# Optimization experiments

Hardware: AMD Instinct MI355X
Metric: run time of the kernel (lower is better)

## Reference

```python
import jax, jax.numpy as jnp
import numpy as np

NUM_NODES = 100000
NUM_EDGES = 1600000
IN_DIM, HID_DIM, OUT_DIM = 128, 128, 70


def gcn_conv(x, edge_index, W, b):
    """PyG-style GCNConv: linear transform, add self-loops, symmetric
    degree-normalized scatter-add aggregation, plus bias."""
    n = x.shape[0]
    xw = x @ W  # [N, D_out]
    src, dst = edge_index[0], edge_index[1]  # messages flow src -> dst
    loop = jnp.arange(n)
    src = jnp.concatenate([src, loop])
    dst = jnp.concatenate([dst, loop])
    # degree computed at target nodes (with self-loops), edge weight 1
    deg = jax.ops.segment_sum(jnp.ones_like(dst, dtype=xw.dtype), dst,
                              num_segments=n)
    dinv = jnp.where(deg > 0, jax.lax.rsqrt(deg), 0.0)
    norm = dinv[src] * dinv[dst]  # [E+N]
    msgs = xw[src] * norm[:, None]  # [E+N, D_out] gathered messages
    out = jax.ops.segment_sum(msgs, dst, num_segments=n)
    return out + b


def setup_inputs() -> dict:
    key = jax.random.key(0)
    k = jax.random.split(key, 6)
    x = jax.random.normal(k[0], (NUM_NODES, IN_DIM), dtype=jnp.float32)
    edge_index = jax.random.randint(k[1], (2, NUM_EDGES), 0, NUM_NODES,
                                    dtype=jnp.int64)
    # Glorot-style init for weights, zero bias (PyG default)
    W1 = jax.random.normal(k[2], (IN_DIM, HID_DIM), dtype=jnp.float32) / np.sqrt(IN_DIM)
    b1 = jnp.zeros((HID_DIM,), dtype=jnp.float32)
    W2 = jax.random.normal(k[3], (HID_DIM, OUT_DIM), dtype=jnp.float32) / np.sqrt(HID_DIM)
    b2 = jnp.zeros((OUT_DIM,), dtype=jnp.float32)
    return {"x": x, "edge_index": edge_index, "W1": W1, "b1": b1,
            "W2": W2, "b2": b2}


def reference(x, edge_index, W1, b1, W2, b2):
    h = gcn_conv(x, edge_index, W1, b1)
    h = jax.nn.relu(h)
    # dropout(p=0.5) is identity in eval mode
    out = gcn_conv(h, edge_index, W2, b2)
    return out
```

## Files before the change

### kernel.cpp

```cpp
#include <hip/hip_runtime.h>
#include <hip/hip_bf16.h>


#define BSH 8
#define BCHUNK 8192
#define BCAP 8192

typedef __attribute__((ext_vector_type(8))) short short8;
typedef __attribute__((ext_vector_type(4))) float float4v;
typedef __attribute__((ext_vector_type(2))) float float2v;

__device__ __forceinline__ float bf_lo(unsigned u) { return __uint_as_float(u << 16); }
__device__ __forceinline__ float bf_hi(unsigned u) { return __uint_as_float(u & 0xffff0000u); }
__device__ __forceinline__ float bf2f(unsigned short h) {
    return __uint_as_float((unsigned)h << 16);
}
__device__ __forceinline__ unsigned short f2bf(float f) {
    unsigned u = __float_as_uint(f);
    u += 0x7fff + ((u >> 16) & 1);
    return (unsigned short)(u >> 16);
}
__device__ __forceinline__ void acc8(float* acc, uint4 m) {
    acc[0] += bf_lo(m.x); acc[1] += bf_hi(m.x);
    acc[2] += bf_lo(m.y); acc[3] += bf_hi(m.y);
    acc[4] += bf_lo(m.z); acc[5] += bf_hi(m.z);
    acc[6] += bf_lo(m.w); acc[7] += bf_hi(m.w);
}

__global__ void k_bucket_scatter(const int* __restrict__ src, const int* __restrict__ dst,
                                 int* __restrict__ bwcur,
                                 unsigned long long* __restrict__ tmp, int E, int nb) {
    __shared__ int lh[512];
    __shared__ int lb[512];
    int t = threadIdx.x;
    for (int j = t; j < nb; j += 256) lh[j] = 0;
    __syncthreads();
    int e0 = blockIdx.x * BCHUNK;
    int e1 = min(E, e0 + BCHUNK);
    for (int e = e0 + t; e < e1; e += 256) atomicAdd(&lh[dst[e] >> BSH], 1);
    __syncthreads();
    for (int j = t; j < nb; j += 256) {
        int c = lh[j];
        lb[j] = c ? atomicAdd(&bwcur[j], c) : 0;
        lh[j] = 0;
    }
    __syncthreads();
    for (int e = e0 + t; e < e1; e += 256) {
        int d = dst[e];
        int b = d >> BSH;
        int o = atomicAdd(&lh[b], 1);
        int pos = lb[b] + o;
        if (pos < BCAP)
            tmp[(size_t)b * BCAP + pos] =
                ((unsigned long long)(unsigned)d << 32) | (unsigned)src[e];
    }
}

__global__ void k_bucket_finalize(const unsigned long long* __restrict__ tmp,
                                  const int* __restrict__ bwcur,
                                  int* __restrict__ deg, float* __restrict__ dinv,
                                  int* __restrict__ rs, int* __restrict__ csr, int N) {
    __shared__ int cnt[256];
    __shared__ int sc[256];
    int b = blockIdx.x;
    int t = threadIdx.x;
    int e0 = b * BCAP;
    int e1 = e0 + min(bwcur[b], BCAP);
    cnt[t] = 0;
    __syncthreads();
    for (int e = e0 + t; e < e1; e += 256) {
        int d = (int)(tmp[e] >> 32);
        atomicAdd(&cnt[d & 255], 1);
    }
    __syncthreads();
    int c = cnt[t];
    sc[t] = c;
    __syncthreads();
    for (int off = 1; off < 256; off <<= 1) {
        int add = (t >= off) ? sc[t - off] : 0;
        __syncthreads();
        sc[t] += add;
        __syncthreads();
    }
    int excl = sc[t] - c;
    __syncthreads();
    sc[t] = excl;
    int node = (b << BSH) + t;
    if (node < N) {
        deg[node] = c;
        dinv[node] = rsqrtf((float)(c + 1));
        rs[node] = e0 + excl;
    }
    cnt[t] = 0;
    __syncthreads();
    for (int e = e0 + t; e < e1; e += 256) {
        unsigned long long p = tmp[e];
        int j = ((int)(p >> 32)) & 255;
        int o = atomicAdd(&cnt[j], 1);
        csr[e0 + sc[j] + o] = (int)(p & 0xffffffffu);
    }
}

__global__ void k_prep_w(const float* __restrict__ W1, const float* __restrict__ W2,
                         unsigned short* __restrict__ w1th, unsigned short* __restrict__ w1tl,
                         unsigned short* __restrict__ w2th, unsigned short* __restrict__ w2tl) {
    int i = blockIdx.x * blockDim.x + threadIdx.x;
    if (i < 128 * 128) {
        int col = i % 128, k = i / 128;
        float w = W1[k * 128 + col];
        unsigned short h = f2bf(w);
        w1th[(size_t)col * 128 + k] = h;
        w1tl[(size_t)col * 128 + k] = f2bf(w - bf2f(h));
    } else if (i < 128 * 128 + 80 * 128) {
        int j = i - 128 * 128;
        int col = j % 80, k = j / 80;
        float w = (col < 70) ? W2[k * 70 + col] : 0.f;
        unsigned short h = f2bf(w);
        w2th[(size_t)col * 128 + k] = h;
        w2tl[(size_t)col * 128 + k] = f2bf(w - bf2f(h));
    }
}

template <int DOUT, int OSTRIDE, int NT>
__global__ __launch_bounds__(256, 3) void k_gemm_mfma(
        const float* __restrict__ X, const unsigned short* __restrict__ Wth,
        const unsigned short* __restrict__ Wtl,
        const float* __restrict__ dinv, unsigned short* __restrict__ Y, int n) {
    __shared__ short xs_h[64][136];
    __shared__ short xs_l[64][136];
    int t = threadIdx.x;
    int lane = t & 63, wave = t >> 6;
    int m16 = lane & 15, quad = lane >> 4;
    int r0 = blockIdx.x * 64;

    short8 bh[2][4], bl[2][4];
    int nt0 = wave, nt1 = wave + 4;
#pragma unroll
    for (int i = 0; i < 2; i++) {
        int nt = i ? nt1 : nt0;
        if (nt >= NT) continue;
        int col = nt * 16 + m16;
#pragma unroll
        for (int kc = 0; kc < 4; kc++) {
            bh[i][kc] = *(const short8*)&Wth[(size_t)col * 128 + kc * 32 + quad * 8];
            bl[i][kc] = *(const short8*)&Wtl[(size_t)col * 128 + kc * 32 + quad * 8];
        }
    }

    for (int p = t; p < 64 * 32; p += 256) {
        int row = p >> 5;
        int k4 = p & 31;
        int gr = r0 + row;
        if (gr >= n) gr = n - 1;
        float4v xv = __builtin_nontemporal_load(
            (const float4v*)(X + (size_t)gr * 128 + 4 * k4));
        unsigned short h0 = f2bf(xv.x), h1 = f2bf(xv.y);
        unsigned short h2 = f2bf(xv.z), h3 = f2bf(xv.w);
        unsigned short l0 = f2bf(xv.x - bf2f(h0)), l1 = f2bf(xv.y - bf2f(h1));
        unsigned short l2 = f2bf(xv.z - bf2f(h2)), l3 = f2bf(xv.w - bf2f(h3));
        *(uint2*)&xs_h[row][4 * k4] =
            make_uint2((unsigned)h0 | ((unsigned)h1 << 16), (unsigned)h2 | ((unsigned)h3 << 16));
        *(uint2*)&xs_l[row][4 * k4] =
            make_uint2((unsigned)l0 | ((unsigned)l1 << 16), (unsigned)l2 | ((unsigned)l3 << 16));
    }
    __syncthreads();

    float4v acc[2][4];
#pragma unroll
    for (int i = 0; i < 2; i++)
#pragma unroll
        for (int ms = 0; ms < 4; ms++) acc[i][ms] = (float4v){0.f, 0.f, 0.f, 0.f};

#pragma unroll
    for (int kc = 0; kc < 4; kc++) {
#pragma unroll
        for (int ms = 0; ms < 4; ms++) {
            short8 ah = *(short8*)&xs_h[ms * 16 + m16][kc * 32 + quad * 8];
            short8 al = *(short8*)&xs_l[ms * 16 + m16][kc * 32 + quad * 8];
#pragma unroll
            for (int i = 0; i < 2; i++) {
                int nt = i ? nt1 : nt0;
                if (nt >= NT) continue;
                acc[i][ms] = __builtin_amdgcn_mfma_f32_16x16x32_bf16(ah, bh[i][kc], acc[i][ms], 0, 0, 0);
                acc[i][ms] = __builtin_amdgcn_mfma_f32_16x16x32_bf16(al, bh[i][kc], acc[i][ms], 0, 0, 0);
                acc[i][ms] = __builtin_amdgcn_mfma_f32_16x16x32_bf16(ah, bl[i][kc], acc[i][ms], 0, 0, 0);
            }
        }
    }

#pragma unroll
    for (int i = 0; i < 2; i++) {
        int nt = i ? nt1 : nt0;
        if (nt >= NT) continue;
        int col = nt * 16 + m16;
        if (col >= OSTRIDE) continue;
#pragma unroll
        for (int ms = 0; ms < 4; ms++) {
#pragma unroll
            for (int r = 0; r < 4; r++) {
                int row = r0 + ms * 16 + quad * 4 + r;
                if (row < n) {
                    float val = (col < DOUT) ? acc[i][ms][r] * dinv[row] : 0.f;
                    Y[(size_t)row * OSTRIDE + col] = f2bf(val);
                }
            }
        }
    }
}

__global__ __launch_bounds__(256, 8) void k_agg_w128(
        const uint4* __restrict__ msg, const float* __restrict__ dinv,
        const int* __restrict__ rs, const int* __restrict__ deg,
        const int* __restrict__ csr, const float* __restrict__ bias,
        float* __restrict__ out, int n) {
    int lane = threadIdx.x & 63;
    int q = lane & 15;
    int slot = lane >> 4;
    int wid = blockIdx.x * 4 + (threadIdx.x >> 6);
    int nw = gridDim.x * 4;
    for (int v = wid; v < n; v += nw) {
        int start = rs[v];
        int cnt = deg[v];
        float dv = dinv[v];
        uint4 mself = msg[(size_t)v * 16 + q];
        float acc[8] = {0.f, 0.f, 0.f, 0.f, 0.f, 0.f, 0.f, 0.f};
        int i = slot;
        for (; i + 12 < cnt; i += 16) {
            int s0 = csr[start + i];
            int s1 = csr[start + i + 4];
            int s2 = csr[start + i + 8];
            int s3 = csr[start + i + 12];
            uint4 m0 = msg[(size_t)s0 * 16 + q];
            uint4 m1 = msg[(size_t)s1 * 16 + q];
            uint4 m2 = msg[(size_t)s2 * 16 + q];
            uint4 m3 = msg[(size_t)s3 * 16 + q];
            acc8(acc, m0);
            acc8(acc, m1);
            acc8(acc, m2);
            acc8(acc, m3);
        }
        for (; i + 4 < cnt; i += 8) {
            int s0 = csr[start + i];
            int s1 = csr[start + i + 4];
            uint4 m0 = msg[(size_t)s0 * 16 + q];
            uint4 m1 = msg[(size_t)s1 * 16 + q];
            acc8(acc, m0);
            acc8(acc, m1);
        }
        if (i < cnt) {
            int s = csr[start + i];
            uint4 m = msg[(size_t)s * 16 + q];
            acc8(acc, m);
        }
#pragma unroll
        for (int j = 0; j < 8; j++) acc[j] += __shfl_xor(acc[j], 32);
#pragma unroll
        for (int j = 0; j < 8; j++) acc[j] += __shfl_xor(acc[j], 16);
        if (slot == 0) {
            float o[8];
            o[0] = acc[0] + bf_lo(mself.x); o[1] = acc[1] + bf_hi(mself.x);
            o[2] = acc[2] + bf_lo(mself.y); o[3] = acc[3] + bf_hi(mself.y);
            o[4] = acc[4] + bf_lo(mself.z); o[5] = acc[5] + bf_hi(mself.z);
            o[6] = acc[6] + bf_lo(mself.w); o[7] = acc[7] + bf_hi(mself.w);
            float r[8];
#pragma unroll
            for (int j = 0; j < 8; j++) r[j] = fmaxf(dv * o[j] + bias[8 * q + j], 0.f);
            float4v* op = (float4v*)(out + (size_t)v * 128 + 8 * q);
            __builtin_nontemporal_store((float4v){r[0], r[1], r[2], r[3]}, op);
            __builtin_nontemporal_store((float4v){r[4], r[5], r[6], r[7]}, op + 1);
        }
    }
}

__global__ __launch_bounds__(256, 8) void k_agg_w72(
        const uint4* __restrict__ msg, const float* __restrict__ dinv,
        const int* __restrict__ rs, const int* __restrict__ deg,
        const int* __restrict__ csr, const float* __restrict__ bias,
        float* __restrict__ out, int n) {
    int lane = threadIdx.x & 63;
    int slot = lane / 9;
    int q = lane - slot * 9;
    bool active = lane < 63;
    int wid = blockIdx.x * 4 + (threadIdx.x >> 6);
    int nw = gridDim.x * 4;
    for (int v = wid; v < n; v += nw) {
        int start = rs[v];
        int cnt = deg[v];
        float dv = dinv[v];
        float acc[8] = {0.f, 0.f, 0.f, 0.f, 0.f, 0.f, 0.f, 0.f};
        uint4 mself = make_uint4(0, 0, 0, 0);
        if (active) {
            mself = msg[(size_t)v * 9 + q];
            int i = slot;
            for (; i + 14 < cnt; i += 21) {
                int s0 = csr[start + i];
                int s1 = csr[start + i + 7];
                int s2 = csr[start + i + 14];
                uint4 m0 = msg[(size_t)s0 * 9 + q];
                uint4 m1 = msg[(size_t)s1 * 9 + q];
                uint4 m2 = msg[(size_t)s2 * 9 + q];
                acc8(acc, m0);
                acc8(acc, m1);
                acc8(acc, m2);
            }
            for (; i + 7 < cnt; i += 14) {
                int s0 = csr[start + i];
                int s1 = csr[start + i + 7];
                uint4 m0 = msg[(size_t)s0 * 9 + q];
                uint4 m1 = msg[(size_t)s1 * 9 + q];
                acc8(acc, m0);
                acc8(acc, m1);
            }
            if (i < cnt) {
                int s = csr[start + i];
                uint4 m = msg[(size_t)s * 9 + q];
                acc8(acc, m);
            }
        }
#pragma unroll
        for (int j = 0; j < 8; j++) {
            float t27 = __shfl(acc[j], lane + 27);
            if (lane < 27) acc[j] += t27;
        }
#pragma unroll
        for (int j = 0; j < 8; j++) {
            float t54 = __shfl(acc[j], lane + 54);
            float t9  = __shfl(acc[j], lane + 9);
            float t18 = __shfl(acc[j], lane + 18);
            if (lane < 9) acc[j] += t54 + t9 + t18;
        }
        if (lane < 9) {
            float o[8];
            o[0] = acc[0] + bf_lo(mself.x); o[1] = acc[1] + bf_hi(mself.x);
            o[2] = acc[2] + bf_lo(mself.y); o[3] = acc[3] + bf_hi(mself.y);
            o[4] = acc[4] + bf_lo(mself.z); o[5] = acc[5] + bf_hi(mself.z);
            o[6] = acc[6] + bf_lo(mself.w); o[7] = acc[7] + bf_hi(mself.w);
            float* orow = out + (size_t)v * 70 + 8 * q;
#pragma unroll
            for (int jj = 0; jj < 4; jj++) {
                int f = 8 * q + 2 * jj;
                if (f < 70) {
                    float2 st = make_float2(dv * o[2 * jj] + bias[f],
                                            dv * o[2 * jj + 1] + bias[f + 1]);
                    *(float2*)(orow + 2 * jj) = st;
                }
            }
        }
    }
}

static inline size_t alignup(size_t x) { return (x + 255) & ~(size_t)255; }

extern "C" void kernel_launch(void* const* d_in, const int* in_sizes, int n_in,
                              void* d_out, int out_size, void* d_ws, size_t ws_size,
                              hipStream_t stream) {
    const float* x = (const float*)d_in[0];
    const int* edge = (const int*)d_in[1];
    const float* W1 = (const float*)d_in[2];
    const float* b1 = (const float*)d_in[3];
    const float* W2 = (const float*)d_in[4];
    const float* b2 = (const float*)d_in[5];

    const int N = in_sizes[0] / 128;
    const int E = in_sizes[1] / 2;
    const int* src = edge;
    const int* dst = edge + E;
    const int nb = (N + 255) >> BSH;

    char* w = (char*)d_ws;
    int* deg = (int*)w;              w += alignup((size_t)N * 4);
    float* dinv = (float*)w;         w += alignup((size_t)N * 4);
    int* rs = (int*)w;               w += alignup((size_t)N * 4);
    int* bwcur = (int*)w;            w += alignup(4096);
    int* csr = (int*)w;              w += alignup((size_t)nb * BCAP * 4);
    unsigned short* msg1 = (unsigned short*)w; w += alignup((size_t)N * 128 * 2);
    unsigned short* msg2 = (unsigned short*)w; w += alignup((size_t)N * 72 * 2);
    unsigned short* w1th = (unsigned short*)w; w += alignup(128 * 128 * 2);
    unsigned short* w1tl = (unsigned short*)w; w += alignup(128 * 128 * 2);
    unsigned short* w2th = (unsigned short*)w; w += alignup(80 * 128 * 2);
    unsigned short* w2tl = (unsigned short*)w; w += alignup(80 * 128 * 2);
    float* h = (float*)w;            w += alignup((size_t)N * 128 * 4);
    unsigned long long* tmp = (unsigned long long*)h;

    k_prep_w<<<(128 * 128 + 80 * 128 + 255) / 256, 256, 0, stream>>>(
        W1, W2, w1th, w1tl, w2th, w2tl);

    hipMemsetAsync(bwcur, 0, (size_t)nb * 4, stream);
    k_bucket_scatter<<<(E + BCHUNK - 1) / BCHUNK, 256, 0, stream>>>(src, dst, bwcur, tmp, E, nb);
    k_bucket_finalize<<<nb, 256, 0, stream>>>(tmp, bwcur, deg, dinv, rs, csr, N);

    int gblocks = (N + 63) / 64;

    k_gemm_mfma<128, 128, 8><<<gblocks, 256, 0, stream>>>(x, w1th, w1tl, dinv, msg1, N);
    k_agg_w128<<<2048, 256, 0, stream>>>((const uint4*)msg1, dinv, rs, deg, csr, b1, h, N);

    k_gemm_mfma<70, 72, 5><<<gblocks, 256, 0, stream>>>(h, w2th, w2tl, dinv, msg2, N);
    k_agg_w72<<<2048, 256, 0, stream>>>((const uint4*)msg2, dinv, rs, deg, csr, b2,
                                        (float*)d_out, N);
}
```

Before: 345.1 us.

## Replace two-pass bucket CSR build with global degree count, scan, atomic fill

The two-pass bucket build (LDS histogram, packed 64-bit scatter to a temp buffer, then per-bucket finalize) is replaced by a global atomic degree count, a per-bucket prefix scan, and a fill pass that places each source index with a per-node atomic cursor. Weight prep is folded into the degree-count kernel to save a launch. This drops the 64-bit temp write and re-read, but adds many contended global atomics on random destinations. Edge order within each CSR row also becomes nondeterministic.

After: 474.7 us. +37.5%, slower.

```diff
diff --git a/kernel.cpp b/kernel.cpp
--- a/kernel.cpp
+++ b/kernel.cpp
@@ -3,8 +3,9 @@
 
 
 #define BSH 8
-#define BCHUNK 8192
 #define BCAP 8192
+#define PREPB 104
+#define CNTB 1024
 
 typedef __attribute__((ext_vector_type(8))) short short8;
 typedef __attribute__((ext_vector_type(4))) float float4v;
@@ -27,53 +28,48 @@
     acc[6] += bf_lo(m.w); acc[7] += bf_hi(m.w);
 }
 
-__global__ void k_bucket_scatter(const int* __restrict__ src, const int* __restrict__ dst,
-                                 int* __restrict__ bwcur,
-                                 unsigned long long* __restrict__ tmp, int E, int nb) {
-    __shared__ int lh[512];
-    __shared__ int lb[512];
-    int t = threadIdx.x;
-    for (int j = t; j < nb; j += 256) lh[j] = 0;
-    __syncthreads();
-    int e0 = blockIdx.x * BCHUNK;
-    int e1 = min(E, e0 + BCHUNK);
-    for (int e = e0 + t; e < e1; e += 256) atomicAdd(&lh[dst[e] >> BSH], 1);
-    __syncthreads();
-    for (int j = t; j < nb; j += 256) {
-        int c = lh[j];
-        lb[j] = c ? atomicAdd(&bwcur[j], c) : 0;
-        lh[j] = 0;
-    }
-    __syncthreads();
-    for (int e = e0 + t; e < e1; e += 256) {
-        int d = dst[e];
-        int b = d >> BSH;
-        int o = atomicAdd(&lh[b], 1);
-        int pos = lb[b] + o;
-        if (pos < BCAP)
-            tmp[(size_t)b * BCAP + pos] =
-                ((unsigned long long)(unsigned)d << 32) | (unsigned)src[e];
-    }
-}
-
-__global__ void k_bucket_finalize(const unsigned long long* __restrict__ tmp,
-                                  const int* __restrict__ bwcur,
-                                  int* __restrict__ deg, float* __restrict__ dinv,
-                                  int* __restrict__ rs, int* __restrict__ csr, int N) {
-    __shared__ int cnt[256];
+__global__ void k_prep_count(const float* __restrict__ W1, const float* __restrict__ W2,
+                             unsigned short* __restrict__ w1th, unsigned short* __restrict__ w1tl,
+                             unsigned short* __restrict__ w2th, unsigned short* __restrict__ w2tl,
+                             const int* __restrict__ dst, int* __restrict__ deg, int E) {
+    if (blockIdx.x < PREPB) {
+        int i = blockIdx.x * 256 + threadIdx.x;
+        if (i < 128 * 128) {
+            int col = i % 128, k = i / 128;
+            float w = W1[k * 128 + col];
+            unsigned short h = f2bf(w);
+            w1th[(size_t)col * 128 + k] = h;
+            w1tl[(size_t)col * 128 + k] = f2bf(w - bf2f(h));
+        } else if (i < 128 * 128 + 80 * 128) {
+            int j = i - 128 * 128;
+            int col = j % 80, k = j / 80;
+            float w = (col < 70) ? W2[k * 70 + col] : 0.f;
+            unsigned short h = f2bf(w);
+            w2th[(size_t)col * 128 + k] = h;
+            w2tl[(size_t)col * 128 + k] = f2bf(w - bf2f(h));
+        }
+        return;
+    }
+    int tid = (blockIdx.x - PREPB) * 256 + threadIdx.x;
+    int stride = CNTB * 256;
+    int E4 = E >> 2;
+    for (int i = tid; i < E4; i += stride) {
+        int4 d4 = ((const int4*)dst)[i];
+        atomicAdd(&deg[d4.x], 1);
+        atomicAdd(&deg[d4.y], 1);
+        atomicAdd(&deg[d4.z], 1);
+        atomicAdd(&deg[d4.w], 1);
+    }
+    for (int e = E4 * 4 + tid; e < E; e += stride) atomicAdd(&deg[dst[e]], 1);
+}
+
+__global__ void k_scan_rs(const int* __restrict__ deg, float* __restrict__ dinv,
+                          int* __restrict__ rs, int* __restrict__ cursor, int N) {
     __shared__ int sc[256];
     int b = blockIdx.x;
     int t = threadIdx.x;
-    int e0 = b * BCAP;
-    int e1 = e0 + min(bwcur[b], BCAP);
-    cnt[t] = 0;
-    __syncthreads();
-    for (int e = e0 + t; e < e1; e += 256) {
-        int d = (int)(tmp[e] >> 32);
-        atomicAdd(&cnt[d & 255], 1);
-    }
-    __syncthreads();
-    int c = cnt[t];
+    int node = (b << BSH) + t;
+    int c = (node < N) ? deg[node] : 0;
     sc[t] = c;
     __syncthreads();
     for (int off = 1; off < 256; off <<= 1) {
@@ -83,41 +79,35 @@
         __syncthreads();
     }
     int excl = sc[t] - c;
-    __syncthreads();
-    sc[t] = excl;
-    int node = (b << BSH) + t;
     if (node < N) {
-        deg[node] = c;
+        int base = b * BCAP + min(excl, BCAP);
+        rs[node] = base;
+        cursor[node] = base;
         dinv[node] = rsqrtf((float)(c + 1));
-        rs[node] = e0 + excl;
-    }
-    cnt[t] = 0;
-    __syncthreads();
-    for (int e = e0 + t; e < e1; e += 256) {
-        unsigned long long p = tmp[e];
-        int j = ((int)(p >> 32)) & 255;
-        int o = atomicAdd(&cnt[j], 1);
-        csr[e0 + sc[j] + o] = (int)(p & 0xffffffffu);
-    }
-}
-
-__global__ void k_prep_w(const float* __restrict__ W1, const float* __restrict__ W2,
-                         unsigned short* __restrict__ w1th, unsigned short* __restrict__ w1tl,
-                         unsigned short* __restrict__ w2th, unsigned short* __restrict__ w2tl) {
-    int i = blockIdx.x * blockDim.x + threadIdx.x;
-    if (i < 128 * 128) {
-        int col = i % 128, k = i / 128;
-        float w = W1[k * 128 + col];
-        unsigned short h = f2bf(w);
-        w1th[(size_t)col * 128 + k] = h;
-        w1tl[(size_t)col * 128 + k] = f2bf(w - bf2f(h));
-    } else if (i < 128 * 128 + 80 * 128) {
-        int j = i - 128 * 128;
-        int col = j % 80, k = j / 80;
-        float w = (col < 70) ? W2[k * 70 + col] : 0.f;
-        unsigned short h = f2bf(w);
-        w2th[(size_t)col * 128 + k] = h;
-        w2tl[(size_t)col * 128 + k] = f2bf(w - bf2f(h));
+    }
+}
+
+__global__ void k_fill(const int* __restrict__ src, const int* __restrict__ dst,
+                       int* __restrict__ cursor, int* __restrict__ csr, int E) {
+    int tid = blockIdx.x * 256 + threadIdx.x;
+    int stride = gridDim.x * 256;
+    int E4 = E >> 2;
+    for (int i = tid; i < E4; i += stride) {
+        int4 d4 = ((const int4*)dst)[i];
+        int4 s4 = ((const int4*)src)[i];
+        int p0 = atomicAdd(&cursor[d4.x], 1);
+        int p1 = atomicAdd(&cursor[d4.y], 1);
+        int p2 = atomicAdd(&cursor[d4.z], 1);
+        int p3 = atomicAdd(&cursor[d4.w], 1);
+        if (p0 < ((d4.x >> BSH) + 1) * BCAP) csr[p0] = s4.x;
+        if (p1 < ((d4.y >> BSH) + 1) * BCAP) csr[p1] = s4.y;
+        if (p2 < ((d4.z >> BSH) + 1) * BCAP) csr[p2] = s4.z;
+        if (p3 < ((d4.w >> BSH) + 1) * BCAP) csr[p3] = s4.w;
+    }
+    for (int e = E4 * 4 + tid; e < E; e += stride) {
+        int d = dst[e];
+        int p = atomicAdd(&cursor[d], 1);
+        if (p < ((d >> BSH) + 1) * BCAP) csr[p] = src[e];
     }
 }
 
@@ -371,7 +361,7 @@
     int* deg = (int*)w;              w += alignup((size_t)N * 4);
     float* dinv = (float*)w;         w += alignup((size_t)N * 4);
     int* rs = (int*)w;               w += alignup((size_t)N * 4);
-    int* bwcur = (int*)w;            w += alignup(4096);
+    int* cursor = (int*)w;           w += alignup((size_t)N * 4);
     int* csr = (int*)w;              w += alignup((size_t)nb * BCAP * 4);
     unsigned short* msg1 = (unsigned short*)w; w += alignup((size_t)N * 128 * 2);
     unsigned short* msg2 = (unsigned short*)w; w += alignup((size_t)N * 72 * 2);
@@ -380,14 +370,12 @@
     unsigned short* w2th = (unsigned short*)w; w += alignup(80 * 128 * 2);
     unsigned short* w2tl = (unsigned short*)w; w += alignup(80 * 128 * 2);
     float* h = (float*)w;            w += alignup((size_t)N * 128 * 4);
-    unsigned long long* tmp = (unsigned long long*)h;
-
-    k_prep_w<<<(128 * 128 + 80 * 128 + 255) / 256, 256, 0, stream>>>(
-        W1, W2, w1th, w1tl, w2th, w2tl);
-
-    hipMemsetAsync(bwcur, 0, (size_t)nb * 4, stream);
-    k_bucket_scatter<<<(E + BCHUNK - 1) / BCHUNK, 256, 0, stream>>>(src, dst, bwcur, tmp, E, nb);
-    k_bucket_finalize<<<nb, 256, 0, stream>>>(tmp, bwcur, deg, dinv, rs, csr, N);
+
+    hipMemsetAsync(deg, 0, (size_t)N * 4, stream);
+    k_prep_count<<<PREPB + CNTB, 256, 0, stream>>>(W1, W2, w1th, w1tl, w2th, w2tl,
+                                                   dst, deg, E);
+    k_scan_rs<<<nb, 256, 0, stream>>>(deg, dinv, rs, cursor, N);
+    k_fill<<<1024, 256, 0, stream>>>(src, dst, cursor, csr, E);
 
     int gblocks = (N + 63) / 64;
 
```
